# Kernel tuning notes

Measured on AMD Instinct MI355X. Metric: run time of the kernel, lower is better.

The kernel has to match this reference:

```python
import jax, jax.numpy as jnp
import numpy as np

B, N, D, H = 32, 8192, 128, 128


def setup_inputs() -> dict:
    key = jax.random.key(0)
    ks = jax.random.split(key, 9)
    s = lambda k, shp, fan: jax.random.normal(k, shp, jnp.float32) / np.sqrt(fan)
    return {
        "x": jax.random.normal(ks[0], (B, N, D), jnp.float32),
        "Wg1": s(ks[1], (D, H), D), "bg1": jnp.zeros((H,), jnp.float32),
        "Wg2": s(ks[2], (H, 1), H), "bg2": jnp.zeros((1,), jnp.float32),
        "Wn1": s(ks[3], (D, H), D), "bn1": jnp.zeros((H,), jnp.float32),
        "Wn2": s(ks[4], (H, H), H), "bn2": jnp.zeros((H,), jnp.float32),
    }


def reference(x, Wg1, bg1, Wg2, bg2, Wn1, bn1, Wn2, bn2):
    # gate_nn: Linear -> SiLU -> Linear(->1); scores per node
    gate = jnp.einsum("bnd,dh->bnh", x, Wg1) + bg1
    gate = jax.nn.silu(gate)
    gate = jnp.einsum("bnh,ho->bno", gate, Wg2) + bg2  # [B,N,1]
    # nn: Linear -> SiLU -> Linear; transformed node features
    h = jax.nn.silu(jnp.einsum("bnd,dh->bnh", x, Wn1) + bn1)
    h = jnp.einsum("bnh,hk->bnk", h, Wn2) + bn2  # [B,N,H]
    # segment softmax over nodes of each graph (segments == batch dim here)
    attn = jax.nn.softmax(gate, axis=1)  # [B,N,1]
    # weighted-sum pooling per graph
    return jnp.sum(attn * h, axis=1)  # [B,H]
```

## Files before the change

kernel.cpp:

```cpp
#include <hip/hip_runtime.h>

#define B_ 32
#define N_ 8192
#define D_ 128
#define H_ 128
#define R_ (B_ * N_)

#define NBLK 4096

typedef _Float16 f16;
typedef __attribute__((ext_vector_type(4))) _Float16 f16x4;
typedef __attribute__((ext_vector_type(8))) _Float16 f16x8;
typedef __attribute__((ext_vector_type(4))) float f32x4;

static constexpr size_t WPACK_OFF = 0;
static constexpr size_t VPART_OFF = 65536;
static constexpr size_t SPART_OFF = VPART_OFF + (size_t)NBLK * 128 * 4;

__device__ __forceinline__ float silu_f(float v) {
    return v * __builtin_amdgcn_rcpf(1.0f + __expf(-v));
}

__device__ __forceinline__ f32x4 mfma16(f16x8 a, f16x8 b, f32x4 c) {
    return __builtin_amdgcn_mfma_f32_16x16x32_f16(a, b, c, 0, 0, 0);
}

__global__ void k0_prepack(const float* __restrict__ Wg1,
                           const float* __restrict__ Wn1,
                           f16* __restrict__ wp) {
    int tid = blockIdx.x * 256 + threadIdx.x;
    int m    = tid >> 14;
    int r    = tid & 16383;
    int j    = r & 7;
    int lane = (r >> 3) & 63;
    int kc   = (r >> 9) & 3;
    int nt   = r >> 11;
    int k = kc * 32 + (lane >> 4) * 8 + j;
    int n = nt * 16 + (lane & 15);
    const float* W = m ? Wn1 : Wg1;
    wp[tid] = (f16)W[k * 128 + n];
}

__global__ __launch_bounds__(512, 4) void k1_fused(
        const float* __restrict__ x,
        const float* __restrict__ bg1, const float* __restrict__ wg2,
        const float* __restrict__ bg2, const float* __restrict__ bn1,
        const f16* __restrict__ wp,
        float* __restrict__ vpart, float* __restrict__ spart) {
    __shared__ f16 xlds[64 * 128];
    __shared__ float gpart[8][64];

    const int tid  = threadIdx.x;
    const int w    = tid >> 6;
    const int lane = tid & 63;
    const int q    = lane >> 4;
    const int c    = lane & 15;

    const long rowbase = (long)blockIdx.x * 64;
    const float4* xg = (const float4*)x + rowbase * 32;
    float4 xv[4];
#pragma unroll
    for (int s = 0; s < 4; ++s) xv[s] = xg[s * 512 + tid];

    const f16x8* wpv = (const f16x8*)wp;
    f16x8 fg1[4], fn1[4];
#pragma unroll
    for (int kc = 0; kc < 4; ++kc) {
        int base = (w * 4 + kc) * 64 + lane;
        fg1[kc] = wpv[base];
        fn1[kc] = wpv[2048 + base];
    }
    float bg1q[4], wg2q[4], bn1q[4];
#pragma unroll
    for (int r = 0; r < 4; ++r) {
        int col = w * 16 + q * 4 + r;
        bg1q[r] = bg1[col];
        wg2q[r] = wg2[col];
        bn1q[r] = bn1[col];
    }
    const float bg2v = bg2[0];

    const int loh_e = (q * 16 + (c ^ q)) * 8;
    const int loh_o = (q * 16 + (c ^ (q | 4))) * 8;

#pragma unroll
    for (int s = 0; s < 4; ++s) {
        int e   = s * 512 + tid;
        int row = e >> 5, c4 = e & 31;
        int mt = row >> 4, cc = row & 15;
        int kc = c4 >> 3, qq = (c4 >> 1) & 3, j = (c4 & 1) * 4;
        int sw = (c4 >> 1) & 7;
        float4 vv = xv[s];
        f16x4 hv = {(f16)vv.x, (f16)vv.y, (f16)vv.z, (f16)vv.w};
        *(f16x4*)&xlds[((mt * 4 + kc) * 64 + qq * 16 + (cc ^ sw)) * 8 + j] = hv;
    }
    __syncthreads();

    f16x4 hq[4];
#pragma unroll
    for (int mt = 0; mt < 4; ++mt) {
        f16x8 a[4];
#pragma unroll
        for (int kc = 0; kc < 4; ++kc)
            a[kc] = *(const f16x8*)&xlds[(mt * 4 + kc) * 512 +
                                         ((kc & 1) ? loh_o : loh_e)];
        f32x4 ag = {0.f, 0.f, 0.f, 0.f};
        f32x4 an = {0.f, 0.f, 0.f, 0.f};
#pragma unroll
        for (int kc = 0; kc < 4; ++kc) {
            ag = mfma16(fg1[kc], a[kc], ag);
            an = mfma16(fn1[kc], a[kc], an);
        }
        f16x4 h4;
#pragma unroll
        for (int r = 0; r < 4; ++r) h4[r] = (f16)silu_f(an[r] + bn1q[r]);
        hq[mt] = h4;
        float p = 0.f;
#pragma unroll
        for (int r = 0; r < 4; ++r)
            p += silu_f(ag[r] + bg1q[r]) * wg2q[r];
        p += __shfl_xor(p, 16);
        p += __shfl_xor(p, 32);
        if (lane < 16) gpart[w][mt * 16 + lane] = p;
    }
    __syncthreads();

    float e4[4];
#pragma unroll
    for (int mt = 0; mt < 4; ++mt) {
        float g = bg2v;
#pragma unroll
        for (int k = 0; k < 8; ++k) g += gpart[k][mt * 16 + c];
        e4[mt] = __expf(g);
    }

    float V[4] = {0.f, 0.f, 0.f, 0.f};
#pragma unroll
    for (int mt = 0; mt < 4; ++mt)
#pragma unroll
        for (int r = 0; r < 4; ++r)
            V[r] += e4[mt] * (float)hq[mt][r];

#pragma unroll
    for (int m = 1; m < 16; m <<= 1)
#pragma unroll
        for (int r = 0; r < 4; ++r) V[r] += __shfl_xor(V[r], m);
    if (c == 0) {
        float4 o = {V[0], V[1], V[2], V[3]};
        *(float4*)&vpart[(long)blockIdx.x * 128 + w * 16 + q * 4] = o;
    }
    if (w == 0) {
        float Sl = e4[0] + e4[1] + e4[2] + e4[3];
#pragma unroll
        for (int m = 1; m < 16; m <<= 1) Sl += __shfl_xor(Sl, m);
        if (lane == 0) spart[blockIdx.x] = Sl;
    }
}

__global__ void k2_combine(const float* __restrict__ vpart,
                           const float* __restrict__ spart,
                           const float* __restrict__ Wn2,
                           const float* __restrict__ bn2,
                           float* __restrict__ out) {
    const int b = blockIdx.x;
    const int t = threadIdx.x;

    __shared__ float pooled[128];
    __shared__ float sred2[2];

    float v = 0.f;
    if (t < 128) {
        const float* vp = vpart + (long)b * 128 * 128;
#pragma unroll 8
        for (int k = 0; k < 128; ++k) v += vp[k * 128 + t];
    }

    float s = (t < 128) ? spart[b * 128 + t] : 0.f;
#pragma unroll
    for (int m = 1; m < 64; m <<= 1) s += __shfl_xor(s, m);
    if (t < 128 && (t & 63) == 0) sred2[t >> 6] = s;
    __syncthreads();

    if (t < 128) pooled[t] = v / (sred2[0] + sred2[1]);
    __syncthreads();
    if (t < 128) {
        float acc = bn2[t];
#pragma unroll 8
        for (int k = 0; k < 128; ++k) acc += pooled[k] * Wn2[k * 128 + t];
        out[b * 128 + t] = acc;
    }
}

extern "C" void kernel_launch(void* const* d_in, const int* in_sizes, int n_in,
                              void* d_out, int out_size, void* d_ws, size_t ws_size,
                              hipStream_t stream) {
    const float* x   = (const float*)d_in[0];
    const float* Wg1 = (const float*)d_in[1];
    const float* bg1 = (const float*)d_in[2];
    const float* Wg2 = (const float*)d_in[3];
    const float* bg2 = (const float*)d_in[4];
    const float* Wn1 = (const float*)d_in[5];
    const float* bn1 = (const float*)d_in[6];
    const float* Wn2 = (const float*)d_in[7];
    const float* bn2 = (const float*)d_in[8];
    float* out = (float*)d_out;

    char* ws = (char*)d_ws;
    f16*   wp    = (f16*)(ws + WPACK_OFF);
    float* vpart = (float*)(ws + VPART_OFF);
    float* spart = (float*)(ws + SPART_OFF);

    k0_prepack<<<128, 256, 0, stream>>>(Wg1, Wn1, wp);
    k1_fused<<<NBLK, 512, 0, stream>>>(x, bg1, Wg2, bg2, bn1, wp, vpart, spart);
    k2_combine<<<32, 256, 0, stream>>>(vpart, spart, Wn2, bn2, out);
}
```

Measured before the change: 222.4 us.

## Process eight row tiles per block with register-prefetched x loads

Each block of the fused kernel now loops over eight 64-row tiles instead of one, cutting the grid from 4096 to 512 blocks. While the current tile is computed, the next tile of x is prefetched into registers, then converted and written to LDS, so global loads overlap compute. V and the softmax denominator accumulate across tiles, and the combine kernel reduces 16 partials per graph instead of 128. The cost is a smaller grid with an extra barrier per tile, which may underfill the CUs or expose load latency.

```diff
diff --git a/kernel.cpp b/kernel.cpp
--- a/kernel.cpp
+++ b/kernel.cpp
@@ -6,7 +6,8 @@
 #define H_ 128
 #define R_ (B_ * N_)
 
-#define NBLK 4096
+#define TILES 8
+#define NBLK 512
 
 typedef _Float16 f16;
 typedef __attribute__((ext_vector_type(4))) _Float16 f16x4;
@@ -56,8 +57,8 @@
     const int q    = lane >> 4;
     const int c    = lane & 15;
 
-    const long rowbase = (long)blockIdx.x * 64;
-    const float4* xg = (const float4*)x + rowbase * 32;
+    const float4* xg = (const float4*)x + (long)blockIdx.x * (64 * TILES) * 32;
+
     float4 xv[4];
 #pragma unroll
     for (int s = 0; s < 4; ++s) xv[s] = xg[s * 512 + tid];
@@ -94,52 +95,79 @@
         f16x4 hv = {(f16)vv.x, (f16)vv.y, (f16)vv.z, (f16)vv.w};
         *(f16x4*)&xlds[((mt * 4 + kc) * 64 + qq * 16 + (cc ^ sw)) * 8 + j] = hv;
     }
+    if (TILES > 1) {
+#pragma unroll
+        for (int s = 0; s < 4; ++s) xv[s] = xg[2048 + s * 512 + tid];
+    }
+
+    float V[4] = {0.f, 0.f, 0.f, 0.f};
+    float Sacc = 0.f;
+
     __syncthreads();
 
-    f16x4 hq[4];
-#pragma unroll
-    for (int mt = 0; mt < 4; ++mt) {
-        f16x8 a[4];
-#pragma unroll
-        for (int kc = 0; kc < 4; ++kc)
-            a[kc] = *(const f16x8*)&xlds[(mt * 4 + kc) * 512 +
-                                         ((kc & 1) ? loh_o : loh_e)];
-        f32x4 ag = {0.f, 0.f, 0.f, 0.f};
-        f32x4 an = {0.f, 0.f, 0.f, 0.f};
-#pragma unroll
-        for (int kc = 0; kc < 4; ++kc) {
-            ag = mfma16(fg1[kc], a[kc], ag);
-            an = mfma16(fn1[kc], a[kc], an);
+#pragma unroll 1
+    for (int t = 0; t < TILES; ++t) {
+        f16x4 hq[4];
+#pragma unroll
+        for (int mt = 0; mt < 4; ++mt) {
+            f16x8 a[4];
+#pragma unroll
+            for (int kc = 0; kc < 4; ++kc)
+                a[kc] = *(const f16x8*)&xlds[(mt * 4 + kc) * 512 +
+                                             ((kc & 1) ? loh_o : loh_e)];
+            f32x4 ag = {0.f, 0.f, 0.f, 0.f};
+            f32x4 an = {0.f, 0.f, 0.f, 0.f};
+#pragma unroll
+            for (int kc = 0; kc < 4; ++kc) {
+                ag = mfma16(fg1[kc], a[kc], ag);
+                an = mfma16(fn1[kc], a[kc], an);
+            }
+            f16x4 h4;
+#pragma unroll
+            for (int r = 0; r < 4; ++r) h4[r] = (f16)silu_f(an[r] + bn1q[r]);
+            hq[mt] = h4;
+            float p = 0.f;
+#pragma unroll
+            for (int r = 0; r < 4; ++r)
+                p += silu_f(ag[r] + bg1q[r]) * wg2q[r];
+            p += __shfl_xor(p, 16);
+            p += __shfl_xor(p, 32);
+            if (lane < 16) gpart[w][mt * 16 + lane] = p;
         }
-        f16x4 h4;
-#pragma unroll
-        for (int r = 0; r < 4; ++r) h4[r] = (f16)silu_f(an[r] + bn1q[r]);
-        hq[mt] = h4;
-        float p = 0.f;
-#pragma unroll
-        for (int r = 0; r < 4; ++r)
-            p += silu_f(ag[r] + bg1q[r]) * wg2q[r];
-        p += __shfl_xor(p, 16);
-        p += __shfl_xor(p, 32);
-        if (lane < 16) gpart[w][mt * 16 + lane] = p;
-    }
-    __syncthreads();
-
-    float e4[4];
-#pragma unroll
-    for (int mt = 0; mt < 4; ++mt) {
-        float g = bg2v;
-#pragma unroll
-        for (int k = 0; k < 8; ++k) g += gpart[k][mt * 16 + c];
-        e4[mt] = __expf(g);
-    }
-
-    float V[4] = {0.f, 0.f, 0.f, 0.f};
-#pragma unroll
-    for (int mt = 0; mt < 4; ++mt)
-#pragma unroll
-        for (int r = 0; r < 4; ++r)
-            V[r] += e4[mt] * (float)hq[mt][r];
+        __syncthreads();
+
+#pragma unroll
+        for (int mt = 0; mt < 4; ++mt) {
+            float g = bg2v;
+#pragma unroll
+            for (int k = 0; k < 8; ++k) g += gpart[k][mt * 16 + c];
+            float e4 = __expf(g);
+            Sacc += e4;
+#pragma unroll
+            for (int r = 0; r < 4; ++r)
+                V[r] += e4 * (float)hq[mt][r];
+        }
+
+        if (t + 1 < TILES) {
+#pragma unroll
+            for (int s = 0; s < 4; ++s) {
+                int e   = s * 512 + tid;
+                int row = e >> 5, c4 = e & 31;
+                int mt = row >> 4, cc = row & 15;
+                int kc = c4 >> 3, qq = (c4 >> 1) & 3, j = (c4 & 1) * 4;
+                int sw = (c4 >> 1) & 7;
+                float4 vv = xv[s];
+                f16x4 hv = {(f16)vv.x, (f16)vv.y, (f16)vv.z, (f16)vv.w};
+                *(f16x4*)&xlds[((mt * 4 + kc) * 64 + qq * 16 + (cc ^ sw)) * 8 + j] = hv;
+            }
+            if (t + 2 < TILES) {
+#pragma unroll
+                for (int s = 0; s < 4; ++s)
+                    xv[s] = xg[(t + 2) * 2048 + s * 512 + tid];
+            }
+            __syncthreads();
+        }
+    }
 
 #pragma unroll
     for (int m = 1; m < 16; m <<= 1)
@@ -150,7 +178,7 @@
         *(float4*)&vpart[(long)blockIdx.x * 128 + w * 16 + q * 4] = o;
     }
     if (w == 0) {
-        float Sl = e4[0] + e4[1] + e4[2] + e4[3];
+        float Sl = Sacc;
 #pragma unroll
         for (int m = 1; m < 16; m <<= 1) Sl += __shfl_xor(Sl, m);
         if (lane == 0) spart[blockIdx.x] = Sl;
@@ -166,22 +194,22 @@
     const int t = threadIdx.x;
 
     __shared__ float pooled[128];
-    __shared__ float sred2[2];
+    __shared__ float sred;
 
     float v = 0.f;
     if (t < 128) {
-        const float* vp = vpart + (long)b * 128 * 128;
-#pragma unroll 8
-        for (int k = 0; k < 128; ++k) v += vp[k * 128 + t];
-    }
-
-    float s = (t < 128) ? spart[b * 128 + t] : 0.f;
-#pragma unroll
-    for (int m = 1; m < 64; m <<= 1) s += __shfl_xor(s, m);
-    if (t < 128 && (t & 63) == 0) sred2[t >> 6] = s;
+        const float* vp = vpart + (long)b * 16 * 128;
+#pragma unroll
+        for (int k = 0; k < 16; ++k) v += vp[k * 128 + t];
+    }
+
+    float s = (t < 16) ? spart[b * 16 + t] : 0.f;
+#pragma unroll
+    for (int m = 1; m < 16; m <<= 1) s += __shfl_xor(s, m);
+    if (t == 0) sred = s;
     __syncthreads();
 
-    if (t < 128) pooled[t] = v / (sred2[0] + sred2[1]);
+    if (t < 128) pooled[t] = v / sred;
     __syncthreads();
     if (t < 128) {
         float acc = bn2[t];
```

New measurement: 235.9 us. 6.1% more time.

## Stage packed weights in LDS and give each wavefront whole rows with persistent blocks

Applied to the files above, without the earlier changes.

Blocks drop from 4096 to 512. Each block loads both packed f16 weight matrices (64KB) plus the biases into LDS once. Each wavefront then handles 64 rows on its own in four 16-row tasks, reading x straight from global memory into MFMA fragments and computing all 128 hidden columns. This removes the per-block x staging through LDS, the cross-wave gate reduction and the second barrier, and spreads the weight load over more rows. The cost is heavy LDS reads of weights per MFMA, a large register accumulator (32 floats of V), less occupancy from the 64KB LDS footprint, and non-coalesced row-wise x loads.

```diff
diff --git a/kernel.cpp b/kernel.cpp
--- a/kernel.cpp
+++ b/kernel.cpp
@@ -6,7 +6,7 @@
 #define H_ 128
 #define R_ (B_ * N_)
 
-#define NBLK 4096
+#define NBLK 512
 
 typedef _Float16 f16;
 typedef __attribute__((ext_vector_type(4))) _Float16 f16x4;
@@ -15,7 +15,7 @@
 
 static constexpr size_t WPACK_OFF = 0;
 static constexpr size_t VPART_OFF = 65536;
-static constexpr size_t SPART_OFF = VPART_OFF + (size_t)NBLK * 128 * 4;
+static constexpr size_t SPART_OFF = VPART_OFF + 4096ull * 128 * 4;
 
 __device__ __forceinline__ float silu_f(float v) {
     return v * __builtin_amdgcn_rcpf(1.0f + __expf(-v));
@@ -47,8 +47,8 @@
         const float* __restrict__ bg2, const float* __restrict__ bn1,
         const f16* __restrict__ wp,
         float* __restrict__ vpart, float* __restrict__ spart) {
-    __shared__ f16 xlds[64 * 128];
-    __shared__ float gpart[8][64];
+    __shared__ f16 wlds[2 * 128 * 128];
+    __shared__ float blds[3 * 128];
 
     const int tid  = threadIdx.x;
     const int w    = tid >> 6;
@@ -56,105 +56,93 @@
     const int q    = lane >> 4;
     const int c    = lane & 15;
 
-    const long rowbase = (long)blockIdx.x * 64;
-    const float4* xg = (const float4*)x + rowbase * 32;
-    float4 xv[4];
-#pragma unroll
-    for (int s = 0; s < 4; ++s) xv[s] = xg[s * 512 + tid];
-
-    const f16x8* wpv = (const f16x8*)wp;
-    f16x8 fg1[4], fn1[4];
-#pragma unroll
-    for (int kc = 0; kc < 4; ++kc) {
-        int base = (w * 4 + kc) * 64 + lane;
-        fg1[kc] = wpv[base];
-        fn1[kc] = wpv[2048 + base];
-    }
-    float bg1q[4], wg2q[4], bn1q[4];
-#pragma unroll
-    for (int r = 0; r < 4; ++r) {
-        int col = w * 16 + q * 4 + r;
-        bg1q[r] = bg1[col];
-        wg2q[r] = wg2[col];
-        bn1q[r] = bn1[col];
+    const float4* wp4 = (const float4*)wp;
+    float4* wl4 = (float4*)wlds;
+#pragma unroll
+    for (int i = 0; i < 8; ++i) wl4[i * 512 + tid] = wp4[i * 512 + tid];
+    if (tid < 128) {
+        blds[tid]       = bg1[tid];
+        blds[128 + tid] = bn1[tid];
+        blds[256 + tid] = wg2[tid];
     }
     const float bg2v = bg2[0];
-
-    const int loh_e = (q * 16 + (c ^ q)) * 8;
-    const int loh_o = (q * 16 + (c ^ (q | 4))) * 8;
-
-#pragma unroll
-    for (int s = 0; s < 4; ++s) {
-        int e   = s * 512 + tid;
-        int row = e >> 5, c4 = e & 31;
-        int mt = row >> 4, cc = row & 15;
-        int kc = c4 >> 3, qq = (c4 >> 1) & 3, j = (c4 & 1) * 4;
-        int sw = (c4 >> 1) & 7;
-        float4 vv = xv[s];
-        f16x4 hv = {(f16)vv.x, (f16)vv.y, (f16)vv.z, (f16)vv.w};
-        *(f16x4*)&xlds[((mt * 4 + kc) * 64 + qq * 16 + (cc ^ sw)) * 8 + j] = hv;
-    }
     __syncthreads();
 
-    f16x4 hq[4];
-#pragma unroll
-    for (int mt = 0; mt < 4; ++mt) {
+    const int wgid = blockIdx.x * 8 + w;
+    const f16x8* wv = (const f16x8*)wlds;
+
+    float V[8][4] = {{0.f,0.f,0.f,0.f},{0.f,0.f,0.f,0.f},{0.f,0.f,0.f,0.f},
+                     {0.f,0.f,0.f,0.f},{0.f,0.f,0.f,0.f},{0.f,0.f,0.f,0.f},
+                     {0.f,0.f,0.f,0.f},{0.f,0.f,0.f,0.f}};
+    float Sacc = 0.f;
+
+#pragma unroll 1
+    for (int task = 0; task < 4; ++task) {
+        const long row0 = (long)wgid * 64 + task * 16 + c;
+        const float4* xr = (const float4*)(x + row0 * 128);
+        float4 xv[8];
+#pragma unroll
+        for (int kc = 0; kc < 4; ++kc) {
+            xv[kc * 2]     = xr[kc * 8 + q * 2];
+            xv[kc * 2 + 1] = xr[kc * 8 + q * 2 + 1];
+        }
         f16x8 a[4];
 #pragma unroll
-        for (int kc = 0; kc < 4; ++kc)
-            a[kc] = *(const f16x8*)&xlds[(mt * 4 + kc) * 512 +
-                                         ((kc & 1) ? loh_o : loh_e)];
-        f32x4 ag = {0.f, 0.f, 0.f, 0.f};
-        f32x4 an = {0.f, 0.f, 0.f, 0.f};
-#pragma unroll
         for (int kc = 0; kc < 4; ++kc) {
-            ag = mfma16(fg1[kc], a[kc], ag);
-            an = mfma16(fn1[kc], a[kc], an);
-        }
-        f16x4 h4;
-#pragma unroll
-        for (int r = 0; r < 4; ++r) h4[r] = (f16)silu_f(an[r] + bn1q[r]);
-        hq[mt] = h4;
+            float4 f0 = xv[kc * 2], f1 = xv[kc * 2 + 1];
+            f16x8 av = {(f16)f0.x, (f16)f0.y, (f16)f0.z, (f16)f0.w,
+                        (f16)f1.x, (f16)f1.y, (f16)f1.z, (f16)f1.w};
+            a[kc] = av;
+        }
+
         float p = 0.f;
-#pragma unroll
-        for (int r = 0; r < 4; ++r)
-            p += silu_f(ag[r] + bg1q[r]) * wg2q[r];
+        f16x4 h[8];
+#pragma unroll
+        for (int st = 0; st < 8; ++st) {
+            float4 bgi = *(const float4*)&blds[st * 16 + q * 4];
+            float4 bni = *(const float4*)&blds[128 + st * 16 + q * 4];
+            float4 wgi = *(const float4*)&blds[256 + st * 16 + q * 4];
+            f32x4 ag = {bgi.x, bgi.y, bgi.z, bgi.w};
+            f32x4 an = {bni.x, bni.y, bni.z, bni.w};
+#pragma unroll
+            for (int kc = 0; kc < 4; ++kc) {
+                ag = mfma16(wv[(st * 4 + kc) * 64 + lane], a[kc], ag);
+                an = mfma16(wv[2048 + (st * 4 + kc) * 64 + lane], a[kc], an);
+            }
+            f16x4 h4;
+#pragma unroll
+            for (int r = 0; r < 4; ++r) h4[r] = (f16)silu_f(an[r]);
+            h[st] = h4;
+            p += silu_f(ag[0]) * wgi.x + silu_f(ag[1]) * wgi.y
+               + silu_f(ag[2]) * wgi.z + silu_f(ag[3]) * wgi.w;
+        }
         p += __shfl_xor(p, 16);
         p += __shfl_xor(p, 32);
-        if (lane < 16) gpart[w][mt * 16 + lane] = p;
-    }
-    __syncthreads();
-
-    float e4[4];
-#pragma unroll
-    for (int mt = 0; mt < 4; ++mt) {
-        float g = bg2v;
-#pragma unroll
-        for (int k = 0; k < 8; ++k) g += gpart[k][mt * 16 + c];
-        e4[mt] = __expf(g);
-    }
-
-    float V[4] = {0.f, 0.f, 0.f, 0.f};
-#pragma unroll
-    for (int mt = 0; mt < 4; ++mt)
-#pragma unroll
-        for (int r = 0; r < 4; ++r)
-            V[r] += e4[mt] * (float)hq[mt][r];
+        float e4 = __expf(p + bg2v);
+        Sacc += e4;
+#pragma unroll
+        for (int st = 0; st < 8; ++st)
+#pragma unroll
+            for (int r = 0; r < 4; ++r)
+                V[st][r] += e4 * (float)h[st][r];
+    }
 
 #pragma unroll
     for (int m = 1; m < 16; m <<= 1)
 #pragma unroll
-        for (int r = 0; r < 4; ++r) V[r] += __shfl_xor(V[r], m);
+        for (int st = 0; st < 8; ++st)
+#pragma unroll
+            for (int r = 0; r < 4; ++r) V[st][r] += __shfl_xor(V[st][r], m);
     if (c == 0) {
-        float4 o = {V[0], V[1], V[2], V[3]};
-        *(float4*)&vpart[(long)blockIdx.x * 128 + w * 16 + q * 4] = o;
-    }
-    if (w == 0) {
-        float Sl = e4[0] + e4[1] + e4[2] + e4[3];
-#pragma unroll
-        for (int m = 1; m < 16; m <<= 1) Sl += __shfl_xor(Sl, m);
-        if (lane == 0) spart[blockIdx.x] = Sl;
-    }
+#pragma unroll
+        for (int st = 0; st < 8; ++st) {
+            float4 o = {V[st][0], V[st][1], V[st][2], V[st][3]};
+            *(float4*)&vpart[(long)wgid * 128 + st * 16 + q * 4] = o;
+        }
+    }
+#pragma unroll
+    for (int m = 1; m < 16; m <<= 1) Sacc += __shfl_xor(Sacc, m);
+    if (lane == 0) spart[wgid] = Sacc;
 }
 
 __global__ void k2_combine(const float* __restrict__ vpart,
```

After: 597.9 us. +168.9%, slower.
